# Kernel optimization log

Measured on AMD Instinct MI355X. Metric: run time of the kernel, lower is better.

The kernel has to match this reference:

```python
import jax, jax.numpy as jnp
import numpy as np

B = 2048        # batch
D_DENSE = 13    # dense input features
F = 7           # number of sparse features
CARD = 10000    # cardinality per sparse feature (== len(tokenizer_values))
E = 64          # embedding dim per feature
D_OUT = 32      # dense arch output size
S_OUT = 32      # sparse arch output size per feature
D_HID = 2 * D_OUT   # DenseArch MLP hidden (output_size*2 per code)
S_HID = 2 * S_OUT   # SparseArch MLP hidden (output_size*2 per code)
CONCAT = D_OUT + F * S_OUT    # 256
P_IN = CONCAT * CONCAT        # 65536, flattened outer product
P_HID = 512


def setup_inputs() -> dict:
    key = jax.random.key(0)
    ks = jax.random.split(key, 18)
    s = 0.05
    return {
        "dense_features": jax.random.normal(ks[0], (B, D_DENSE), dtype=jnp.float32),
        "sparse_features": jax.random.randint(ks[1], (B, F), 0, CARD, dtype=jnp.int64),
        # tokenizer_values per feature (shared arange, as in metadata)
        "tokenizers": jnp.arange(CARD, dtype=jnp.int64),
        # embedding tables stacked over features: [F, CARD, E]
        "emb_tables": jax.random.normal(ks[2], (F, CARD, E), dtype=jnp.float32) * s,
        # DenseArch MLP
        "dw1": jax.random.normal(ks[3], (D_DENSE, D_HID), dtype=jnp.float32) * s,
        "db1": jnp.zeros((D_HID,), dtype=jnp.float32),
        "dw2": jax.random.normal(ks[4], (D_HID, D_OUT), dtype=jnp.float32) * s,
        "db2": jnp.zeros((D_OUT,), dtype=jnp.float32),
        # per-feature sparse MLPs stacked over features
        "sw1": jax.random.normal(ks[5], (F, E, S_HID), dtype=jnp.float32) * s,
        "sb1": jnp.zeros((F, S_HID), dtype=jnp.float32),
        "sw2": jax.random.normal(ks[6], (F, S_HID, S_OUT), dtype=jnp.float32) * s,
        "sb2": jnp.zeros((F, S_OUT), dtype=jnp.float32),
        # PredictionLayer MLP
        "pw1": jax.random.normal(ks[7], (P_IN, P_HID), dtype=jnp.float32) * s,
        "pb1": jnp.zeros((P_HID,), dtype=jnp.float32),
        "pw2": jax.random.normal(ks[8], (P_HID, 1), dtype=jnp.float32) * s,
        "pb2": jnp.zeros((1,), dtype=jnp.float32),
    }


def reference(dense_features, sparse_features, tokenizers, emb_tables,
              dw1, db1, dw2, db2, sw1, sb1, sw2, sb2, pw1, pb1, pw2, pb2):
    # DenseArch: MLP(13 -> 64 -> 32)
    dense_out = jnp.maximum(dense_features @ dw1 + db1, 0.0) @ dw2 + db2  # [B, D_OUT]

    # SparseArch: equality-match argmax indexing (faithful to get_indices),
    # then embedding gather and per-feature MLP, vectorized over features.
    matches = sparse_features[:, :, None] == tokenizers[None, None, :]  # [B, F, CARD]
    idx = jnp.argmax(matches, axis=2)                                   # [B, F]
    gathered = emb_tables[jnp.arange(emb_tables.shape[0])[None, :], idx]  # [B, F, E]
    h = jnp.maximum(jnp.einsum('bfe,feh->bfh', gathered, sw1) + sb1, 0.0)
    sparse_out = jnp.einsum('bfh,fho->bfo', h, sw2) + sb2                # [B, F, S_OUT]

    # DenseSparseInteractionLayer: concat -> outer product -> flatten
    concat = jnp.concatenate(
        [dense_out, sparse_out.reshape(sparse_out.shape[0], -1)], axis=1)  # [B, CONCAT]
    outer = jnp.einsum('bi,bj->bij', concat, concat)
    flattened = outer.reshape(concat.shape[0], -1)                       # [B, CONCAT^2]

    # PredictionLayer: MLP(CONCAT^2 -> P_HID -> 1) + sigmoid, squeeze
    logits = jnp.maximum(flattened @ pw1 + pb1, 0.0) @ pw2 + pb2
    return jax.nn.sigmoid(logits).squeeze()
```

## Files before the change

kernel.cpp:

```cpp
#include <hip/hip_runtime.h>
#include <hip/hip_fp16.h>
#include <math.h>

#define BATCH 2048
#define NFEAT 7
#define CARD 10000
#define CONCAT 256
#define P_HID 512

#define BM 128
#define BN 128
#define BK 64
#define KSPLIT 12
#define NUNITS 640
#define UNIT_ST (512 * 64)
#define PREP_BLOCKS (NUNITS * 2)

using f16x4   = __attribute__((ext_vector_type(4))) _Float16;
using half8   = __attribute__((ext_vector_type(8))) _Float16;
using floatx4 = __attribute__((ext_vector_type(4))) float;

__device__ __forceinline__ void dma16(const _Float16* g, _Float16* l) {
    __builtin_amdgcn_global_load_lds(
        (const __attribute__((address_space(1))) unsigned int*)g,
        (__attribute__((address_space(3))) unsigned int*)l,
        16, 0, 0);
}

__device__ __forceinline__ void unit_decode(int u, int& i, int& jw) {
    if (u < 256)      { i = u;                jw = u >> 6; }
    else if (u < 448) { int v = u - 256; i = v / 3;        jw = 1 + v % 3; }
    else if (u < 576) { int v = u - 448; i = 64 + (v >> 1); jw = 2 + (v & 1); }
    else              { i = 128 + (u - 576); jw = 3; }
}

__device__ __forceinline__ int split_t0(int ks)     { return ks * 53 + (ks < 4 ? ks : 4); }
__device__ __forceinline__ int split_ntiles(int ks) { return 53 + (ks < 4 ? 1 : 0); }

__global__ __launch_bounds__(256) void fused_pre(
    const float* __restrict__ dense, const int* __restrict__ sparse,
    const float* __restrict__ emb,
    const float* __restrict__ dw1, const float* __restrict__ db1,
    const float* __restrict__ dw2, const float* __restrict__ db2,
    const float* __restrict__ sw1, const float* __restrict__ sb1,
    const float* __restrict__ sw2, const float* __restrict__ sb2,
    const float* __restrict__ pw1,
    _Float16* __restrict__ cbf, _Float16* __restrict__ St)
{
    __shared__ __align__(16) _Float16 sh[64 * 256];
    const int tid = threadIdx.x;

    if (blockIdx.x < PREP_BLOCKS) {
        const int u = blockIdx.x >> 1, nh = blockIdx.x & 1;
        const int nb = nh * 256;
        int i, jw;
        unit_decode(u, i, jw);

#pragma unroll
        for (int m = 0; m < 16; ++m) {
            const int flat = m * 256 + tid;
            const int q = flat >> 6, c4 = flat & 63;
            const int j = (jw << 6) + q;
            floatx4 s = {0.f, 0.f, 0.f, 0.f};
            if (j >= i) {
                s = __builtin_nontemporal_load(
                    (const floatx4*)(pw1 + ((size_t)i * 256 + j) * P_HID + nb + 4 * c4));
                if (j > i) {
                    const floatx4 mv = __builtin_nontemporal_load(
                        (const floatx4*)(pw1 + ((size_t)j * 256 + i) * P_HID + nb + 4 * c4));
                    s += mv;
                }
            }
            f16x4 hv = {(_Float16)s.x, (_Float16)s.y, (_Float16)s.z, (_Float16)s.w};
            *(f16x4*)(sh + q * 256 + 4 * c4) = hv;
        }
        __syncthreads();

        const _Float16* col = sh + tid;
        _Float16* outp = St + (size_t)u * UNIT_ST + (size_t)(nb + tid) * 64;
#pragma unroll
        for (int e = 0; e < 8; ++e) {
            half8 o;
#pragma unroll
            for (int r = 0; r < 8; ++r) o[r] = col[(8 * e + r) * 256];
            *(half8*)(outp + 8 * e) = o;
        }
    } else {
        float* smem = (float*)sh;
        const int wv = tid >> 6, t = tid & 63;
        const int b = (blockIdx.x - PREP_BLOCKS) * 4 + wv;
        float* xs   = smem + wv * 13;
        float* bufA = smem + 64  + wv * 64;
        float* bufB = smem + 320 + wv * 64;

        if (t < 13) xs[t] = dense[b * 13 + t];
        __syncthreads();

        float h = db1[t];
#pragma unroll
        for (int d = 0; d < 13; ++d) h += xs[d] * dw1[d * 64 + t];
        bufA[t] = fmaxf(h, 0.f);
        __syncthreads();

        if (t < 32) {
            float o = db2[t];
#pragma unroll
            for (int k = 0; k < 64; ++k) o += bufA[k] * dw2[k * 32 + t];
            cbf[b * 256 + t] = (_Float16)o;
        }

        for (int f = 0; f < NFEAT; ++f) {
            __syncthreads();
            const int idx = sparse[b * NFEAT + f];
            bufB[t] = emb[((size_t)(f * CARD + idx)) * 64 + t];
            __syncthreads();
            float s = sb1[f * 64 + t];
#pragma unroll
            for (int e = 0; e < 64; ++e) s += bufB[e] * sw1[(f * 64 + e) * 64 + t];
            bufA[t] = fmaxf(s, 0.f);
            __syncthreads();
            if (t < 32) {
                float o = sb2[f * 32 + t];
#pragma unroll
                for (int k = 0; k < 64; ++k) o += bufA[k] * sw2[(f * 64 + k) * 32 + t];
                cbf[b * 256 + 32 + f * 32 + t] = (_Float16)o;
            }
        }
    }
}

__global__ __launch_bounds__(256, 3) void bilinear_gemm(
    const _Float16* __restrict__ cbf, const _Float16* __restrict__ St,
    _Float16* __restrict__ hidpart)
{
    __shared__ _Float16 Al[BM][BK + 8];
    __shared__ _Float16 Bl[BN][BK];

    const int b = blockIdx.x;
    const int xcd = b & 7, slot = b >> 3;
    const int mt = slot & 15;
    const int slice = ((slot >> 4) << 3) | xcd;
    const int nt = slice & 3, ks = slice >> 2;
    const int m0 = mt * BM, n0 = nt * BN;
    const int t0 = split_t0(ks);
    const int ntiles = split_ntiles(ks);

    const int tid = threadIdx.x, lane = tid & 63, wv = tid >> 6;
    const int wrow = (wv & 1) * 64, wcol = (wv >> 1) * 64;
    const int arow = tid >> 1, ajoff = (tid & 1) * 32;

    floatx4 acc[4][4];
#pragma unroll
    for (int i = 0; i < 4; ++i)
#pragma unroll
        for (int j = 0; j < 4; ++j) acc[i][j] = (floatx4){0.f, 0.f, 0.f, 0.f};

    const _Float16* crow = cbf + (m0 + arow) * 256;

    half8 pre[4][4];
#pragma unroll
    for (int jw = 0; jw < 4; ++jw)
#pragma unroll
        for (int x = 0; x < 4; ++x)
            pre[jw][x] = *(const half8*)(crow + (jw << 6) + ajoff + 8 * x);

    const int drow = wv * 32 + (lane >> 3);
    const int eswz = (lane & 7) ^ ((lane >> 3) & 7);
    const _Float16* bsrc = St + (size_t)t0 * UNIT_ST + (size_t)(n0 + drow) * 64 + eswz * 8;
    _Float16* bdst = &Bl[wv * 32][0];

    int ui_c, ujw_c;
    unit_decode(t0, ui_c, ujw_c);
    _Float16 ci_c = crow[ui_c];

    for (int it = 0; it < ntiles; ++it) {
#pragma unroll
        for (int p = 0; p < 4; ++p)
            dma16(bsrc + (size_t)(p * 8) * 64, bdst + (p * 8) * BK);
        bsrc += UNIT_ST;

        {
            const half8 civ = {ci_c, ci_c, ci_c, ci_c, ci_c, ci_c, ci_c, ci_c};
            _Float16* dst = &Al[arow][ajoff];
#define AGEN(JW)                                                         \
            { *(half8*)(dst +  0) = pre[JW][0] * civ;                    \
              *(half8*)(dst +  8) = pre[JW][1] * civ;                    \
              *(half8*)(dst + 16) = pre[JW][2] * civ;                    \
              *(half8*)(dst + 24) = pre[JW][3] * civ; }
            switch (ujw_c) {
                case 0:  AGEN(0); break;
                case 1:  AGEN(1); break;
                case 2:  AGEN(2); break;
                default: AGEN(3); break;
            }
#undef AGEN
        }
        __syncthreads();

        if (it + 1 < ntiles) {
            unit_decode(t0 + it + 1, ui_c, ujw_c);
            ci_c = crow[ui_c];
        }

#pragma unroll
        for (int kk = 0; kk < BK; kk += 32) {
            half8 af[4], bfr[4];
#pragma unroll
            for (int i = 0; i < 4; ++i)
                af[i] = *(const half8*)&Al[wrow + i * 16 + (lane & 15)][kk + (lane >> 4) * 8];
#pragma unroll
            for (int j = 0; j < 4; ++j) {
                const int s = (((kk >> 3) + (lane >> 4)) ^ (lane & 7)) * 8;
                bfr[j] = *(const half8*)&Bl[wcol + j * 16 + (lane & 15)][s];
            }
#pragma unroll
            for (int i = 0; i < 4; ++i)
#pragma unroll
                for (int j = 0; j < 4; ++j)
                    acc[i][j] = __builtin_amdgcn_mfma_f32_16x16x32_f16(
                        af[i], bfr[j], acc[i][j], 0, 0, 0);
        }
        __syncthreads();
    }

    _Float16* outp = hidpart + (size_t)ks * BATCH * P_HID;
    const int r0 = m0 + wrow + (lane >> 4) * 4;
    const int c0 = n0 + wcol + (lane & 15);
#pragma unroll
    for (int i = 0; i < 4; ++i)
#pragma unroll
        for (int j = 0; j < 4; ++j)
#pragma unroll
            for (int r = 0; r < 4; ++r)
                outp[(size_t)(r0 + i * 16 + r) * P_HID + c0 + j * 16] =
                    (_Float16)acc[i][j][r];
}

__global__ __launch_bounds__(256) void finalize(
    const _Float16* __restrict__ hidpart,
    const float* __restrict__ pb1,
    const float* __restrict__ pw2,
    const float* __restrict__ pb2,
    float* __restrict__ out)
{
    const int b = blockIdx.x, t = threadIdx.x;
    const int wv = t >> 6, lane = t & 63;

    float acc[8];
#pragma unroll
    for (int k = 0; k < 8; ++k) acc[k] = 0.f;

#pragma unroll
    for (int si = 0; si < 3; ++si) {
        const int s = wv + 4 * si;
        const half8 v = *(const half8*)(hidpart + (size_t)s * BATCH * P_HID
                                        + (size_t)b * P_HID + lane * 8);
#pragma unroll
        for (int k = 0; k < 8; ++k) acc[k] += (float)v[k];
    }

    __shared__ float red[4 * 512];
#pragma unroll
    for (int k = 0; k < 8; ++k) red[wv * 512 + k * 64 + lane] = acc[k];
    __syncthreads();

    if (wv == 0) {
        float dot = 0.f;
#pragma unroll
        for (int k = 0; k < 8; ++k) {
            const int n = lane * 8 + k;
            float v = red[k * 64 + lane] + red[512 + k * 64 + lane]
                    + red[1024 + k * 64 + lane] + red[1536 + k * 64 + lane];
            v += pb1[n];
            v = fmaxf(v, 0.f);
            dot += v * pw2[n];
        }
#pragma unroll
        for (int off = 32; off; off >>= 1) dot += __shfl_down(dot, off, 64);
        if (lane == 0) {
            const float s = dot + pb2[0];
            out[b] = 1.f / (1.f + expf(-s));
        }
    }
}

extern "C" void kernel_launch(void* const* d_in, const int* in_sizes, int n_in,
                              void* d_out, int out_size, void* d_ws, size_t ws_size,
                              hipStream_t stream)
{
    const float* dense  = (const float*)d_in[0];
    const int*   sparse = (const int*)d_in[1];
    const float* emb = (const float*)d_in[3];
    const float* dw1 = (const float*)d_in[4];
    const float* db1 = (const float*)d_in[5];
    const float* dw2 = (const float*)d_in[6];
    const float* db2 = (const float*)d_in[7];
    const float* sw1 = (const float*)d_in[8];
    const float* sb1 = (const float*)d_in[9];
    const float* sw2 = (const float*)d_in[10];
    const float* sb2 = (const float*)d_in[11];
    const float* pw1 = (const float*)d_in[12];
    const float* pb1 = (const float*)d_in[13];
    const float* pw2 = (const float*)d_in[14];
    const float* pb2 = (const float*)d_in[15];

    char* ws = (char*)d_ws;
    _Float16* cbf     = (_Float16*)ws;
    _Float16* St      = (_Float16*)(ws + (1 << 20));
    _Float16* hidpart = (_Float16*)(ws + (1 << 20) + ((size_t)40 << 20));

    fused_pre<<<PREP_BLOCKS + BATCH / 4, 256, 0, stream>>>(
        dense, sparse, emb, dw1, db1, dw2, db2, sw1, sb1, sw2, sb2, pw1,
        cbf, St);
    bilinear_gemm<<<16 * 4 * KSPLIT, 256, 0, stream>>>(cbf, St, hidpart);
    finalize<<<BATCH, 256, 0, stream>>>(hidpart, pb1, pw2, pb2, (float*)d_out);
}
```

Before: 349.3 us.

## Double-buffer B tile DMA and XOR-swizzle A tile in bilinear GEMM

Double-buffers the B-operand LDS tile so the global-to-LDS DMA for the next K tile is issued before the current tile is computed, waiting with explicit vmcnt counters in place of full syncthreads. The A tile loses its padding and uses an XOR swizzle to avoid LDS bank conflicts. Wave priority is raised around the MFMA loop. This doubles the B LDS footprint, which may lower occupancy at the 3-blocks-per-CU launch bound, and the hand-written waitcnt depends on the exact count of outstanding loads.

```diff
diff --git a/kernel.cpp b/kernel.cpp
--- a/kernel.cpp
+++ b/kernel.cpp
@@ -133,8 +133,8 @@
     const _Float16* __restrict__ cbf, const _Float16* __restrict__ St,
     _Float16* __restrict__ hidpart)
 {
-    __shared__ _Float16 Al[BM][BK + 8];
-    __shared__ _Float16 Bl[BN][BK];
+    __shared__ __align__(16) _Float16 Al[BM * BK];
+    __shared__ _Float16 Bl[2][BN][BK];
 
     const int b = blockIdx.x;
     const int xcd = b & 7, slot = b >> 3;
@@ -147,6 +147,7 @@
 
     const int tid = threadIdx.x, lane = tid & 63, wv = tid >> 6;
     const int wrow = (wv & 1) * 64, wcol = (wv >> 1) * 64;
+    const int l15 = lane & 15, l4 = lane >> 4, l7 = lane & 7;
     const int arow = tid >> 1, ajoff = (tid & 1) * 32;
 
     floatx4 acc[4][4];
@@ -163,30 +164,40 @@
 #pragma unroll
         for (int x = 0; x < 4; ++x)
             pre[jw][x] = *(const half8*)(crow + (jw << 6) + ajoff + 8 * x);
+
+    char* awbase = (char*)Al + arow * 128;
+    const int awsz = (arow & 7) << 4;
 
     const int drow = wv * 32 + (lane >> 3);
     const int eswz = (lane & 7) ^ ((lane >> 3) & 7);
     const _Float16* bsrc = St + (size_t)t0 * UNIT_ST + (size_t)(n0 + drow) * 64 + eswz * 8;
-    _Float16* bdst = &Bl[wv * 32][0];
 
     int ui_c, ujw_c;
     unit_decode(t0, ui_c, ujw_c);
     _Float16 ci_c = crow[ui_c];
+#pragma unroll
+    for (int p = 0; p < 4; ++p)
+        dma16(bsrc + (size_t)(p * 8) * 64, &Bl[0][wv * 32 + p * 8][0]);
+    bsrc += UNIT_ST;
 
     for (int it = 0; it < ntiles; ++it) {
-#pragma unroll
-        for (int p = 0; p < 4; ++p)
-            dma16(bsrc + (size_t)(p * 8) * 64, bdst + (p * 8) * BK);
-        bsrc += UNIT_ST;
+        const int cur = it & 1;
+        const bool more = (it + 1 < ntiles);
+
+        if (more) {
+#pragma unroll
+            for (int p = 0; p < 4; ++p)
+                dma16(bsrc + (size_t)(p * 8) * 64, &Bl[cur ^ 1][wv * 32 + p * 8][0]);
+            bsrc += UNIT_ST;
+        }
 
         {
             const half8 civ = {ci_c, ci_c, ci_c, ci_c, ci_c, ci_c, ci_c, ci_c};
-            _Float16* dst = &Al[arow][ajoff];
-#define AGEN(JW)                                                         \
-            { *(half8*)(dst +  0) = pre[JW][0] * civ;                    \
-              *(half8*)(dst +  8) = pre[JW][1] * civ;                    \
-              *(half8*)(dst + 16) = pre[JW][2] * civ;                    \
-              *(half8*)(dst + 24) = pre[JW][3] * civ; }
+#define AGEN(JW)                                                              \
+            { *(half8*)(awbase + ((ajoff * 2 +  0) ^ awsz)) = pre[JW][0] * civ; \
+              *(half8*)(awbase + ((ajoff * 2 + 16) ^ awsz)) = pre[JW][1] * civ; \
+              *(half8*)(awbase + ((ajoff * 2 + 32) ^ awsz)) = pre[JW][2] * civ; \
+              *(half8*)(awbase + ((ajoff * 2 + 48) ^ awsz)) = pre[JW][3] * civ; }
             switch (ujw_c) {
                 case 0:  AGEN(0); break;
                 case 1:  AGEN(1); break;
@@ -195,24 +206,33 @@
             }
 #undef AGEN
         }
-        __syncthreads();
-
-        if (it + 1 < ntiles) {
-            unit_decode(t0 + it + 1, ui_c, ujw_c);
-            ci_c = crow[ui_c];
-        }
-
-#pragma unroll
-        for (int kk = 0; kk < BK; kk += 32) {
+
+        if (more) {
+            int ui_n, ujw_n;
+            unit_decode(t0 + it + 1, ui_n, ujw_n);
+            ujw_c = ujw_n;
+            ci_c = crow[ui_n];
+        }
+
+        if (more) asm volatile("s_waitcnt vmcnt(5) lgkmcnt(0)" ::: "memory");
+        else      asm volatile("s_waitcnt vmcnt(0) lgkmcnt(0)" ::: "memory");
+        __builtin_amdgcn_s_barrier();
+        __builtin_amdgcn_sched_barrier(0);
+
+        __builtin_amdgcn_s_setprio(1);
+#pragma unroll
+        for (int kh = 0; kh < 2; ++kh) {
             half8 af[4], bfr[4];
 #pragma unroll
-            for (int i = 0; i < 4; ++i)
-                af[i] = *(const half8*)&Al[wrow + i * 16 + (lane & 15)][kk + (lane >> 4) * 8];
-#pragma unroll
-            for (int j = 0; j < 4; ++j) {
-                const int s = (((kk >> 3) + (lane >> 4)) ^ (lane & 7)) * 8;
-                bfr[j] = *(const half8*)&Bl[wcol + j * 16 + (lane & 15)][s];
+            for (int i = 0; i < 4; ++i) {
+                const int r = wrow + i * 16 + l15;
+                const int cb = (kh * 64 + l4 * 16) ^ ((r & 7) << 4);
+                af[i] = *(const half8*)((const char*)Al + r * 128 + cb);
             }
+            const int s = ((kh * 4 + l4) ^ l7) * 8;
+#pragma unroll
+            for (int j = 0; j < 4; ++j)
+                bfr[j] = *(const half8*)&Bl[cur][wcol + j * 16 + l15][s];
 #pragma unroll
             for (int i = 0; i < 4; ++i)
 #pragma unroll
@@ -220,12 +240,15 @@
                     acc[i][j] = __builtin_amdgcn_mfma_f32_16x16x32_f16(
                         af[i], bfr[j], acc[i][j], 0, 0, 0);
         }
-        __syncthreads();
+        __builtin_amdgcn_s_setprio(0);
+
+        __builtin_amdgcn_sched_barrier(0);
+        __builtin_amdgcn_s_barrier();
     }
 
     _Float16* outp = hidpart + (size_t)ks * BATCH * P_HID;
-    const int r0 = m0 + wrow + (lane >> 4) * 4;
-    const int c0 = n0 + wcol + (lane & 15);
+    const int r0 = m0 + wrow + l4 * 4;
+    const int c0 = n0 + wcol + l15;
 #pragma unroll
     for (int i = 0; i < 4; ++i)
 #pragma unroll
```

Result: no change. 345.8 us, median of 2 (-1.0%).
